# Performance work log

Hardware: AMD Instinct MI355X
Metric: run time of the kernel (lower is better)

Reference implementation:

```python
import jax, jax.numpy as jnp
import numpy as np

B, C, N = 32, 1, 4096
H, W = 64, 64
K, D = 1024, 256  # codebook size, embedding dim


def setup_inputs() -> dict:
    key = jax.random.key(0)
    k0, k1 = jax.random.split(key)
    indices = jax.random.randint(k0, (B, C, N), 0, K, dtype=jnp.int64)
    embedding = jax.random.normal(k1, (K, D), dtype=jnp.float32)
    return {"indices": indices, "embedding": embedding, "h": H, "w": W}


def reference(indices, embedding, h, w):
    b, c, n = indices.shape
    flat = indices.reshape(b * c * n)
    # one-hot @ embedding  ==  direct gather (same math, memory-bound form)
    z_q = jnp.take(embedding, flat, axis=0)        # (b*c*n, D)
    z_q = z_q.reshape(b, h, w, embedding.shape[1])  # view(shape)
    z_q = jnp.transpose(z_q, (0, 3, 1, 2))          # permute(0,3,1,2)
    return z_q
```

## Files before the change

### kernel.cpp

```cpp
#include <hip/hip_runtime.h>


#define VQ_B 32
#define VQ_N 4096
#define VQ_D 256

__global__ __launch_bounds__(256) void vq_gather_kernel(
    const int* __restrict__ indices,
    const float* __restrict__ embedding,
    float* __restrict__ out)
{
    const int bid = blockIdx.x;
    const int b  = bid >> 6;
    const int n0 = (bid & 63) << 6;
    const int l  = threadIdx.x & 63;
    const int w  = threadIdx.x >> 6;

    const int n   = n0 + l;
    const int idx = indices[b * VQ_N + n];
    const float4* __restrict__ row = (const float4*)(embedding + idx * VQ_D);

    const int out_base = b * (VQ_D * VQ_N) + n;

    #pragma unroll
    for (int i = 0; i < 16; ++i) {
        const int c = i * 4 + w;
        const float4 v = row[c];
        const int d = c << 2;
        out[out_base + (d + 0) * VQ_N] = v.x;
        out[out_base + (d + 1) * VQ_N] = v.y;
        out[out_base + (d + 2) * VQ_N] = v.z;
        out[out_base + (d + 3) * VQ_N] = v.w;
    }
}

extern "C" void kernel_launch(void* const* d_in, const int* in_sizes, int n_in,
                              void* d_out, int out_size, void* d_ws, size_t ws_size,
                              hipStream_t stream) {
    const int*   indices   = (const int*)d_in[0];
    const float* embedding = (const float*)d_in[1];
    float* out = (float*)d_out;

    vq_gather_kernel<<<dim3(VQ_B * (VQ_N / 64)), dim3(256), 0, stream>>>(
        indices, embedding, out);
}
```

Before: 143.2 us.

## Stage codebook column slice in LDS and gather with coalesced float4 stores

Each block now handles one batch and a 16-wide slice of the embedding dimension. It loads that slice for all 1024 codebook rows into a swizzled LDS buffer, then gathers from LDS by index and writes contiguous float4 runs of the transposed output. This replaces scattered strided scalar stores with fully coalesced vector stores and moves the random-row gather into LDS. The cost is that the whole codebook slice is reloaded by every block, each block uses 64KB of LDS, and only 512 blocks of 1024 threads are launched.

```diff
diff --git a/kernel.cpp b/kernel.cpp
--- a/kernel.cpp
+++ b/kernel.cpp
@@ -4,33 +4,55 @@
 #define VQ_B 32
 #define VQ_N 4096
 #define VQ_D 256
+#define DC   16
 
-__global__ __launch_bounds__(256) void vq_gather_kernel(
+__device__ __forceinline__ int lds_idx(int r, int dl) {
+    return (r << 4) + (((r >> 1) ^ dl) & 15);
+}
+
+__global__ __launch_bounds__(1024, 8) void vq_lds_gather_kernel(
     const int* __restrict__ indices,
     const float* __restrict__ embedding,
     float* __restrict__ out)
 {
-    const int bid = blockIdx.x;
-    const int b  = bid >> 6;
-    const int n0 = (bid & 63) << 6;
-    const int l  = threadIdx.x & 63;
-    const int w  = threadIdx.x >> 6;
+    __shared__ float lds[1024 * DC];
 
-    const int n   = n0 + l;
-    const int idx = indices[b * VQ_N + n];
-    const float4* __restrict__ row = (const float4*)(embedding + idx * VQ_D);
+    const int b  = blockIdx.x >> 4;
+    const int d0 = (blockIdx.x & 15) * DC;
+    const int t  = threadIdx.x;
 
-    const int out_base = b * (VQ_D * VQ_N) + n;
+    {
+        const int k  = t & 3;
+        const int r0 = t >> 2;
+        #pragma unroll
+        for (int i = 0; i < 4; ++i) {
+            const int r = r0 + i * 256;
+            const float4 v = *(const float4*)(embedding + r * VQ_D + d0 + k * 4);
+            const int dl = k * 4;
+            lds[lds_idx(r, dl + 0)] = v.x;
+            lds[lds_idx(r, dl + 1)] = v.y;
+            lds[lds_idx(r, dl + 2)] = v.z;
+            lds[lds_idx(r, dl + 3)] = v.w;
+        }
+    }
+    __syncthreads();
 
-    #pragma unroll
-    for (int i = 0; i < 16; ++i) {
-        const int c = i * 4 + w;
-        const float4 v = row[c];
-        const int d = c << 2;
-        out[out_base + (d + 0) * VQ_N] = v.x;
-        out[out_base + (d + 1) * VQ_N] = v.y;
-        out[out_base + (d + 2) * VQ_N] = v.z;
-        out[out_base + (d + 3) * VQ_N] = v.w;
+    const int w  = t >> 6;
+    const int l  = t & 63;
+    const int dd = w;
+
+    const int4* __restrict__ idx4 = (const int4*)(indices + b * VQ_N);
+    float* __restrict__ orow = out + b * (VQ_D * VQ_N) + (d0 + w) * VQ_N;
+
+    #pragma unroll 4
+    for (int c = 0; c < VQ_N / 256; ++c) {
+        const int4 id = idx4[c * 64 + l];
+        float4 v;
+        v.x = lds[lds_idx(id.x, dd)];
+        v.y = lds[lds_idx(id.y, dd)];
+        v.z = lds[lds_idx(id.z, dd)];
+        v.w = lds[lds_idx(id.w, dd)];
+        *(float4*)(orow + c * 256 + l * 4) = v;
     }
 }
 
@@ -41,6 +63,6 @@
     const float* embedding = (const float*)d_in[1];
     float* out = (float*)d_out;
 
-    vq_gather_kernel<<<dim3(VQ_B * (VQ_N / 64)), dim3(256), 0, stream>>>(
+    vq_lds_gather_kernel<<<dim3(VQ_B * (VQ_D / DC)), dim3(1024), 0, stream>>>(
         indices, embedding, out);
 }
```

New measurement: 165.9 us. 15.8% more time.
